# Optimization experiments

Measured on AMD Instinct MI355X. Metric: run time of the kernel, lower is better.

Reference implementation:

```python
import jax, jax.numpy as jnp
import numpy as np

K = 1024  # init kwarg k


def setup_inputs() -> dict:
    key = jax.random.key(0)
    k1, k2 = jax.random.split(key)
    B, N, F = 8, 50000, 256
    node_embs = jax.random.normal(k1, (B, N, F), dtype=jnp.float32)
    mask = jnp.zeros((B, N), dtype=jnp.float32)  # additive mask (0 = keep)
    stdv = 1.0 / np.sqrt(F)
    scorer = jax.random.uniform(k2, (F, 1), dtype=jnp.float32, minval=-stdv, maxval=stdv)
    return {"node_embs": node_embs, "mask": mask, "scorer": scorer}


def reference(node_embs, mask, scorer):
    # scores: [B, N] = node_embs @ scorer / ||scorer||, plus additive mask
    scores = jnp.einsum('bnf,f->bn', node_embs, scorer[:, 0]) / jnp.linalg.norm(scorer)
    scores = scores + mask
    # top-k over node dim
    vals, topk_idx = jax.lax.top_k(scores, K)  # [B, K]
    # gather selected node embeddings and scale by tanh of their scores
    gathered = jnp.take_along_axis(node_embs, topk_idx[:, :, None], axis=1)  # [B, K, F]
    gate = jnp.tanh(jnp.take_along_axis(scores, topk_idx, axis=1))  # [B, K]
    out = gathered * gate[:, :, None]
    return out.transpose(0, 2, 1)  # [B, F, K]
```

## Files before the change

kernel.cpp:

```cpp
#include <hip/hip_runtime.h>
#include <math.h>

#define BB 8
#define NN 50000
#define FF 256
#define KK 1024
#define CHUNK 400
#define NCHUNK 125

__device__ __forceinline__ unsigned long long key64(double x) {
    unsigned long long u = (unsigned long long)__double_as_longlong(x);
    u ^= (u & 0x8000000000000000ull) ? 0xFFFFFFFFFFFFFFFFull : 0x8000000000000000ull;
    return u;
}
__device__ __forceinline__ double key_to_double(unsigned long long k) {
    unsigned long long u = (k & 0x8000000000000000ull) ? (k ^ 0x8000000000000000ull) : ~k;
    return __longlong_as_double((long long)u);
}

__global__ __launch_bounds__(1024) void zero_kernel(unsigned int* __restrict__ p, int n) {
    int i = blockIdx.x * 1024 + threadIdx.x;
    if (i < n) p[i] = 0u;
}

__global__ __launch_bounds__(256) void score_kernel(const float* __restrict__ emb,
                                                    const float* __restrict__ mask,
                                                    const float* __restrict__ scorer,
                                                    double* __restrict__ scores,
                                                    unsigned int* __restrict__ ghist) {
    const int b    = blockIdx.x / NCHUNK;
    const int c    = blockIdx.x % NCHUNK;
    const int n0   = c * CHUNK;
    const int lane = threadIdx.x & 63;
    const int wave = threadIdx.x >> 6;

    __shared__ unsigned int h[2048];
    __shared__ float smask[CHUNK];
    for (int i = threadIdx.x; i < 2048; i += 256) h[i] = 0u;
    for (int i = threadIdx.x; i < CHUNK; i += 256) smask[i] = mask[b * NN + n0 + i];
    __syncthreads();

    float4 sc = ((const float4*)scorer)[lane];
    double n2 = (double)sc.x * sc.x + (double)sc.y * sc.y +
                (double)sc.z * sc.z + (double)sc.w * sc.w;
    #pragma unroll
    for (int off = 32; off; off >>= 1) n2 += __shfl_xor(n2, off, 64);
    const double inv_norm = 1.0 / sqrt(n2);

    const float* base  = emb + ((long)b * NN + n0) * FF;
    double*      sbase = scores + (long)b * NN + n0;

    for (int it = 0; it < CHUNK / 16; ++it) {
        const int nn = it * 16 + wave * 4;
        double d[4];
        #pragma unroll
        for (int j = 0; j < 4; j++) {
            float4 v = ((const float4*)(base + (nn + j) * FF))[lane];
            d[j] = (double)v.x * sc.x + (double)v.y * sc.y +
                   (double)v.z * sc.z + (double)v.w * sc.w;
        }
        #pragma unroll
        for (int off = 32; off; off >>= 1) {
            #pragma unroll
            for (int j = 0; j < 4; j++) d[j] += __shfl_xor(d[j], off, 64);
        }
        if (lane == 0) {
            double s[4];
            #pragma unroll
            for (int j = 0; j < 4; j++) {
                s[j] = d[j] * inv_norm + (double)smask[nn + j];
                atomicAdd(&h[(unsigned)(key64(s[j]) >> 53)], 1u);
            }
            *(double2*)(sbase + nn)     = make_double2(s[0], s[1]);
            *(double2*)(sbase + nn + 2) = make_double2(s[2], s[3]);
        }
    }
    __syncthreads();

    unsigned int* gh = ghist + b * 2048;
    for (int i = threadIdx.x; i < 2048; i += 256) {
        unsigned int v = h[i];
        if (v) atomicAdd(&gh[i], v);
    }
}

__global__ __launch_bounds__(1024) void select_kernel(const double* __restrict__ scores,
                                                      const unsigned int* __restrict__ ghist,
                                                      int* __restrict__ topk_idx,
                                                      float* __restrict__ gate) {
    const int b   = blockIdx.x;
    const int tid = threadIdx.x;
    const double* sc = scores + (long)b * NN;

    __shared__ unsigned int h[2048];
    __shared__ unsigned long long keyA[4096];
    __shared__ int idxA[4096];
    __shared__ int bin1_s, need2_s, bin2_s;
    __shared__ unsigned int cnt;

    const int i0 = tid, i1 = tid + 1024;

    h[i0] = ghist[b * 2048 + i0];
    h[i1] = ghist[b * 2048 + i1];
    if (tid == 0) cnt = 0u;
    __syncthreads();

    for (int off = 1; off < 2048; off <<= 1) {
        unsigned a0 = (i0 + off < 2048) ? h[i0 + off] : 0u;
        unsigned a1 = (i1 + off < 2048) ? h[i1 + off] : 0u;
        __syncthreads();
        h[i0] += a0; h[i1] += a1;
        __syncthreads();
    }
    if (h[i0] >= (unsigned)KK && (i0 == 2047 || h[i0 + 1] < (unsigned)KK)) {
        bin1_s = i0; need2_s = KK - (int)((i0 == 2047) ? 0u : h[i0 + 1]);
    }
    if (h[i1] >= (unsigned)KK && (i1 == 2047 || h[i1 + 1] < (unsigned)KK)) {
        bin1_s = i1; need2_s = KK - (int)((i1 == 2047) ? 0u : h[i1 + 1]);
    }
    __syncthreads();
    const unsigned long long bin1 = (unsigned long long)bin1_s;
    const unsigned need2 = (unsigned)need2_s;

    h[i0] = 0u; h[i1] = 0u;
    __syncthreads();
    for (int i = tid; i < NN / 2; i += 1024) {
        double2 v = ((const double2*)sc)[i];
        unsigned long long k0 = key64(v.x), k1 = key64(v.y);
        if ((k0 >> 53) == bin1) atomicAdd(&h[(unsigned)((k0 >> 42) & 2047ull)], 1u);
        if ((k1 >> 53) == bin1) atomicAdd(&h[(unsigned)((k1 >> 42) & 2047ull)], 1u);
    }
    __syncthreads();

    for (int off = 1; off < 2048; off <<= 1) {
        unsigned a0 = (i0 + off < 2048) ? h[i0 + off] : 0u;
        unsigned a1 = (i1 + off < 2048) ? h[i1 + off] : 0u;
        __syncthreads();
        h[i0] += a0; h[i1] += a1;
        __syncthreads();
    }
    if (h[i0] >= need2 && (i0 == 2047 || h[i0 + 1] < need2)) bin2_s = i0;
    if (h[i1] >= need2 && (i1 == 2047 || h[i1 + 1] < need2)) bin2_s = i1;
    __syncthreads();
    const unsigned long long pfx = (bin1 << 11) | (unsigned long long)bin2_s;

    for (int i = tid; i < NN / 2; i += 1024) {
        double2 v = ((const double2*)sc)[i];
        unsigned long long k0 = key64(v.x), k1 = key64(v.y);
        if ((k0 >> 42) >= pfx) {
            unsigned p = atomicAdd(&cnt, 1u);
            if (p < 4096u) { keyA[p] = k0; idxA[p] = 2 * i; }
        }
        if ((k1 >> 42) >= pfx) {
            unsigned p = atomicAdd(&cnt, 1u);
            if (p < 4096u) { keyA[p] = k1; idxA[p] = 2 * i + 1; }
        }
    }
    __syncthreads();
    const int M = (int)(cnt < 4096u ? cnt : 4096u);

    for (int i = tid; i < M; i += 1024) {
        const unsigned long long ki = keyA[i];
        const int ii = idxA[i];
        int rank = 0;
        for (int j = 0; j < M; ++j) {
            const unsigned long long kj = keyA[j];
            rank += (kj > ki) || (kj == ki && idxA[j] < ii);
        }
        if (rank < KK) {
            topk_idx[b * KK + rank] = ii;
            gate[b * KK + rank]     = tanhf((float)key_to_double(ki));
        }
    }
}

__global__ __launch_bounds__(256) void gather_kernel(const float* __restrict__ emb,
                                                     const int* __restrict__ topk_idx,
                                                     const float* __restrict__ gate,
                                                     float* __restrict__ out) {
    const int b  = blockIdx.x >> 5;
    const int kt = blockIdx.x & 31;
    const int k0 = kt * 32;
    const int tid = threadIdx.x;

    __shared__ float tile[32][FF + 4];
    __shared__ int   s_idx[32];
    __shared__ float s_gate[32];

    if (tid < 32) {
        s_idx[tid]  = topk_idx[b * KK + k0 + tid];
        s_gate[tid] = gate[b * KK + k0 + tid];
    }
    __syncthreads();

    const int g = tid >> 6, lane = tid & 63;
    #pragma unroll
    for (int i = 0; i < 8; i++) {
        int kl = i * 4 + g;
        int row = s_idx[kl];
        float gt = s_gate[kl];
        float4 v = ((const float4*)(emb + ((long)b * NN + row) * FF))[lane];
        float* t = &tile[kl][lane * 4];
        t[0] = v.x * gt; t[1] = v.y * gt; t[2] = v.z * gt; t[3] = v.w * gt;
    }
    __syncthreads();

    const long outbase = ((long)b * FF) * KK + k0;
    #pragma unroll
    for (int c = 0; c < 32; c++) {
        int linear = c * 256 + tid;
        int f = linear >> 5;
        int k = linear & 31;
        out[outbase + (long)f * KK + k] = tile[k][f];
    }
}

extern "C" void kernel_launch(void* const* d_in, const int* in_sizes, int n_in,
                              void* d_out, int out_size, void* d_ws, size_t ws_size,
                              hipStream_t stream) {
    const float* emb    = (const float*)d_in[0];
    const float* mask   = (const float*)d_in[1];
    const float* scorer = (const float*)d_in[2];
    float* out = (float*)d_out;

    char* wsb = (char*)d_ws;
    double*       scores  = (double*)wsb;
    unsigned int* ghist   = (unsigned int*)(wsb + sizeof(double) * BB * NN);
    int*          topkidx = (int*)((char*)ghist + sizeof(unsigned int) * BB * 2048);
    float*        gatep   = (float*)((char*)topkidx + sizeof(int) * BB * KK);

    zero_kernel<<<16, 1024, 0, stream>>>(ghist, BB * 2048);
    score_kernel<<<BB * NCHUNK, 256, 0, stream>>>(emb, mask, scorer, scores, ghist);
    select_kernel<<<BB, 1024, 0, stream>>>(scores, ghist, topkidx, gatep);
    gather_kernel<<<BB * 32, 256, 0, stream>>>(emb, topkidx, gatep, out);
}
```

Baseline: 720.1 us.

## Split rows across 16-lane groups and software-pipeline embedding loads in score kernel

The score kernel now assigns one row to each 16-lane group instead of a whole wave per row. Each lane keeps 16 scorer values as doubles and reduces over 4 shuffle steps instead of 6. The loop double-buffers the float4 loads so the next row's data is fetched while the current dot product runs. This targets memory latency and shuffle overhead in a bandwidth-bound pass, at the cost of more registers.

```diff
diff --git a/kernel.cpp b/kernel.cpp
--- a/kernel.cpp
+++ b/kernel.cpp
@@ -7,6 +7,7 @@
 #define KK 1024
 #define CHUNK 400
 #define NCHUNK 125
+#define NIT (CHUNK / 16)
 
 __device__ __forceinline__ unsigned long long key64(double x) {
     unsigned long long u = (unsigned long long)__double_as_longlong(x);
@@ -33,6 +34,9 @@
     const int n0   = c * CHUNK;
     const int lane = threadIdx.x & 63;
     const int wave = threadIdx.x >> 6;
+    const int s    = lane & 15;
+    const int g    = lane >> 4;
+    const int r0   = wave * 4 + g;
 
     __shared__ unsigned int h[2048];
     __shared__ float smask[CHUNK];
@@ -40,47 +44,64 @@
     for (int i = threadIdx.x; i < CHUNK; i += 256) smask[i] = mask[b * NN + n0 + i];
     __syncthreads();
 
-    float4 sc = ((const float4*)scorer)[lane];
-    double n2 = (double)sc.x * sc.x + (double)sc.y * sc.y +
-                (double)sc.z * sc.z + (double)sc.w * sc.w;
-    #pragma unroll
-    for (int off = 32; off; off >>= 1) n2 += __shfl_xor(n2, off, 64);
+    double scd[16];
+    {
+        float4 f0 = ((const float4*)scorer)[s];
+        float4 f1 = ((const float4*)scorer)[s + 16];
+        float4 f2 = ((const float4*)scorer)[s + 32];
+        float4 f3 = ((const float4*)scorer)[s + 48];
+        scd[0]  = f0.x; scd[1]  = f0.y; scd[2]  = f0.z; scd[3]  = f0.w;
+        scd[4]  = f1.x; scd[5]  = f1.y; scd[6]  = f1.z; scd[7]  = f1.w;
+        scd[8]  = f2.x; scd[9]  = f2.y; scd[10] = f2.z; scd[11] = f2.w;
+        scd[12] = f3.x; scd[13] = f3.y; scd[14] = f3.z; scd[15] = f3.w;
+    }
+    double n2 = 0.0;
+    #pragma unroll
+    for (int e = 0; e < 16; ++e) n2 += scd[e] * scd[e];
+    #pragma unroll
+    for (int off = 8; off; off >>= 1) n2 += __shfl_xor(n2, off, 64);
     const double inv_norm = 1.0 / sqrt(n2);
 
     const float* base  = emb + ((long)b * NN + n0) * FF;
     double*      sbase = scores + (long)b * NN + n0;
 
-    for (int it = 0; it < CHUNK / 16; ++it) {
-        const int nn = it * 16 + wave * 4;
-        double d[4];
-        #pragma unroll
-        for (int j = 0; j < 4; j++) {
-            float4 v = ((const float4*)(base + (nn + j) * FF))[lane];
-            d[j] = (double)v.x * sc.x + (double)v.y * sc.y +
-                   (double)v.z * sc.z + (double)v.w * sc.w;
-        }
-        #pragma unroll
-        for (int off = 32; off; off >>= 1) {
-            #pragma unroll
-            for (int j = 0; j < 4; j++) d[j] += __shfl_xor(d[j], off, 64);
-        }
-        if (lane == 0) {
-            double s[4];
-            #pragma unroll
-            for (int j = 0; j < 4; j++) {
-                s[j] = d[j] * inv_norm + (double)smask[nn + j];
-                atomicAdd(&h[(unsigned)(key64(s[j]) >> 53)], 1u);
-            }
-            *(double2*)(sbase + nn)     = make_double2(s[0], s[1]);
-            *(double2*)(sbase + nn + 2) = make_double2(s[2], s[3]);
-        }
-    }
-    __syncthreads();
-
+    auto step = [&](int it, const float4* vv) {
+        double d = 0.0;
+        #pragma unroll
+        for (int i2 = 0; i2 < 4; ++i2) {
+            d += (double)vv[i2].x * scd[4 * i2 + 0] + (double)vv[i2].y * scd[4 * i2 + 1] +
+                 (double)vv[i2].z * scd[4 * i2 + 2] + (double)vv[i2].w * scd[4 * i2 + 3];
+        }
+        #pragma unroll
+        for (int off = 8; off; off >>= 1) d += __shfl_xor(d, off, 64);
+        if (s == 0) {
+            const int row = it * 16 + r0;
+            double sv = d * inv_norm + (double)smask[row];
+            sbase[row] = sv;
+            atomicAdd(&h[(unsigned)(key64(sv) >> 53)], 1u);
+        }
+    };
+
+    const float* rp = base + r0 * FF;
+    float4 v[4], w[4];
+    #pragma unroll
+    for (int i = 0; i < 4; ++i) v[i] = ((const float4*)rp)[s + 16 * i];
+
+    for (int it = 0; it < NIT - 1; ++it) {
+        rp += 16 * FF;
+        #pragma unroll
+        for (int i = 0; i < 4; ++i) w[i] = ((const float4*)rp)[s + 16 * i];
+        step(it, v);
+        #pragma unroll
+        for (int i = 0; i < 4; ++i) v[i] = w[i];
+    }
+    step(NIT - 1, v);
+
+    __syncthreads();
     unsigned int* gh = ghist + b * 2048;
     for (int i = threadIdx.x; i < 2048; i += 256) {
-        unsigned int v = h[i];
-        if (v) atomicAdd(&gh[i], v);
+        unsigned int vv = h[i];
+        if (vv) atomicAdd(&gh[i], vv);
     }
 }
 
```

Result: no change. 713.3 us (-1.0%).
